# Optimization experiments

Measured on AMD Instinct MI355X. Metric: run time of the kernel, lower is better.

The kernel has to match this reference:

```python
import jax, jax.numpy as jnp
import numpy as np

B, T, N, D, H = 64, 100, 1000, 128, 8
DK = D // H
TANH_CLIP = 10.0  # standard attention-model logit clipping


def setup_inputs() -> dict:
    key = jax.random.key(0)
    ks = jax.random.split(key, 7)
    embeddings = jax.random.normal(ks[0], (B, N, D), jnp.float32)
    Wkvl = jax.random.normal(ks[1], (D, 3 * D), jnp.float32) * 0.05   # project_node_embeddings
    Wfixed = jax.random.normal(ks[2], (D, D), jnp.float32) * 0.05     # project_fixed_context
    Wctx = jax.random.normal(ks[3], (D, D), jnp.float32) * 0.05       # env context projection
    Wout = jax.random.normal(ks[4], (D, D), jnp.float32) * 0.05       # glimpse output projection
    idx = jax.random.randint(ks[5], (T, B), 0, N, jnp.int32)          # current node per decode step
    action_mask = jax.random.uniform(ks[6], (T, B, N)) > 0.2          # True = feasible
    action_mask = action_mask.at[..., 0].set(True)                    # >=1 feasible action per row
    return {"embeddings": embeddings, "Wkvl": Wkvl, "Wfixed": Wfixed,
            "Wctx": Wctx, "Wout": Wout, "idx": idx, "action_mask": action_mask}


def reference(embeddings, Wkvl, Wfixed, Wctx, Wout, idx, action_mask):
    # ---- _precompute ----
    graph_ctx = embeddings.mean(axis=1) @ Wfixed                      # [B, D]
    gk, gv, lk = jnp.split(embeddings @ Wkvl, 3, axis=-1)             # each [B, N, D]

    # ---- all T decode steps batched (dynamic embeddings are zero / static env) ----
    # NOTE: the source overwrites glimpse_key with glimpse_val (glimpse_key = cached.glimpse_val + dyn)
    # and calls logit_attention(query, glimpse_key, glimpse_key, ...), so keys == values == gv.
    cur = jnp.take_along_axis(embeddings, idx.T[..., None], axis=1)   # [B, T, D] current node embed
    query = graph_ctx[:, None, :] + cur @ Wctx                        # [B, T, D]

    q = query.reshape(B, T, H, DK).transpose(0, 2, 1, 3)              # [B, H, T, dk]
    k = gv.reshape(B, N, H, DK).transpose(0, 2, 1, 3)                 # [B, H, N, dk]
    v = k                                                             # keys == values per source

    infeasible = ~action_mask.transpose(1, 0, 2)                      # [B, T, N]

    # glimpse (inner) attention, masked
    compat = jnp.einsum('bhtd,bhnd->bhtn', q, k) / jnp.sqrt(jnp.float32(DK))
    compat = jnp.where(infeasible[:, None], -jnp.inf, compat)
    attn = jax.nn.softmax(compat, axis=-1)                            # [B, H, T, N]
    glimpse = jnp.einsum('bhtn,bhnd->bthd', attn, v).reshape(B, T, D) @ Wout  # [B, T, D]

    # pointer logits with tanh clipping
    logits = jnp.einsum('btd,bnd->btn', glimpse, lk) / jnp.sqrt(jnp.float32(D))
    logits = TANH_CLIP * jnp.tanh(logits)
    logits = jnp.where(infeasible, -jnp.inf, logits)
    return jax.nn.log_softmax(logits, axis=-1)                        # [B, T, N]
```

## Files before the change

kernel.cpp:

```cpp
#include <hip/hip_runtime.h>
#include <math.h>

#define B_  64
#define T_  100
#define N_  1000
#define NP_ 1024
#define TP_ 112
#define D_  128
#define H_  8
#define DK_ 16

#define NEG_BIG (-1e30f)

#define OFF_GVH  0
#define OFF_LKH  16777216
#define OFF_GVT  33554432
#define OFF_CTX  50331648
#define OFF_QH   50364416
#define OFF_GPH  52199424
#define OFF_WT   53837824
#define OFF_WV   53870592
#define OFF_WCT  53936128
#define OFF_PART 53968896
#define OFF_PM   54231040
#define OFF_OPT  55148544
#define OFF_LP   62488576

typedef __attribute__((ext_vector_type(8))) short short8;
typedef __attribute__((ext_vector_type(4))) short bs4;
typedef __attribute__((ext_vector_type(4))) float f32x4;

#if __has_builtin(__builtin_amdgcn_mfma_f32_16x16x16bf16_1k)
#define MFMA16(a, b, c) __builtin_amdgcn_mfma_f32_16x16x16bf16_1k(a, b, c, 0, 0, 0)
#else
__device__ __forceinline__ f32x4 mfma16_asm(bs4 a, bs4 b, f32x4 c) {
    f32x4 d;
    asm volatile("v_mfma_f32_16x16x16_bf16 %0, %1, %2, %3"
                 : "=v"(d) : "v"(a), "v"(b), "v"(c));
    return d;
}
#define MFMA16(a, b, c) mfma16_asm(a, b, c)
#endif

__device__ __forceinline__ unsigned int f2bf(float f) {
    unsigned int u = __float_as_uint(f);
    return (u + 0x7fffu + ((u >> 16) & 1u)) >> 16;
}
__device__ __forceinline__ unsigned int packbf(float a, float b) {
    return f2bf(a) | (f2bf(b) << 16);
}
__device__ __forceinline__ float bf2f(unsigned short u) {
    return __uint_as_float(((unsigned int)u) << 16);
}

__global__ __launch_bounds__(256) void pre_kernel(
        const float* __restrict__ Wkvl, const float* __restrict__ Wout,
        const float* __restrict__ Wctx, const float* __restrict__ emb,
        const unsigned char* __restrict__ am,
        unsigned short* __restrict__ wv, unsigned short* __restrict__ wt,
        unsigned short* __restrict__ wct, float* __restrict__ part,
        unsigned long long* __restrict__ pm) {
    __shared__ float p2[256];
    int bx = blockIdx.x;
    int tid = threadIdx.x;
    if (bx < 256) {
        int i = bx * 256 + tid;
        if (i < 32768) {
            int n = i >> 7, k = i & 127;
            wv[i] = (unsigned short)f2bf(Wkvl[k * 384 + 128 + n]);
        } else if (i < 49152) {
            int j = i - 32768;
            wt[j] = (unsigned short)f2bf(Wout[(j & 127) * D_ + (j >> 7)]);
        } else {
            int j = i - 49152;
            wct[j] = (unsigned short)f2bf(Wctx[(j & 127) * D_ + (j >> 7)]);
        }
    } else if (bx < 768) {
        int b2 = bx - 256;
        int b = b2 >> 3, c = b2 & 7;
        int d = tid & 127, half = tid >> 7;
        int nstart = c * 125 + (half ? 63 : 0);
        int ncnt = half ? 62 : 63;
        const float* e = emb + ((size_t)b * N_ + nstart) * D_ + d;
        float s = 0.f;
        for (int n = 0; n < ncnt; ++n) s += e[(size_t)n * D_];
        p2[tid] = s;
        __syncthreads();
        if (half == 0) part[((size_t)b * 8 + c) * D_ + d] = p2[d] + p2[d + 128];
    } else {
        int rid = bx - 768;
        int t = rid >> 6;
        int wvx = tid >> 6, lane = tid & 63;
        const unsigned char* amrow = am + (size_t)rid * N_;
        unsigned long long* pmrow = pm + (size_t)rid * 16;
        #pragma unroll
        for (int i = 0; i < 4; ++i) {
            int c = wvx * 4 + i;
            int n = c * 64 + lane;
            unsigned char v = (t < T_ && n < N_) ? amrow[n] : (unsigned char)0;
            unsigned long long mb = __ballot(v != 0);
            if (lane == 0) pmrow[c] = mb;
        }
    }
}

__global__ __launch_bounds__(128) void ctxb_kernel(
        const float* __restrict__ part, const float* __restrict__ Wfixed,
        float* __restrict__ ctx) {
    __shared__ float mean[D_];
    int b = blockIdx.x;
    int d = threadIdx.x;
    float s = 0.f;
    for (int c = 0; c < 8; ++c) s += part[((size_t)b * 8 + c) * D_ + d];
    mean[d] = s * (1.0f / N_);
    __syncthreads();
    float acc = 0.f;
    for (int k = 0; k < D_; ++k) acc += mean[k] * Wfixed[k * D_ + d];
    ctx[b * D_ + d] = acc;
}

__global__ __launch_bounds__(256) void proj_kernel(
        const float* __restrict__ emb, const unsigned short* __restrict__ wv,
        unsigned short* __restrict__ gvh, unsigned short* __restrict__ lkh,
        unsigned short* __restrict__ gvT) {
    __shared__ unsigned short As[64 * 136];
    __shared__ unsigned short Gs[64 * 130];
    int rb = blockIdx.x;
    int tid = threadIdx.x;
    int w = tid >> 6, lane = tid & 63, col = lane & 15, quad = lane >> 4;
    const float* a0 = emb + (size_t)rb * 64 * D_;
    #pragma unroll
    for (int i = 0; i < 8; ++i) {
        int idx = tid + i * 256;
        int r = idx >> 5, kq = idx & 31;
        float4 f = *(const float4*)(a0 + r * D_ + kq * 4);
        *(uint2*)&As[r * 136 + kq * 4] = make_uint2(packbf(f.x, f.y), packbf(f.z, f.w));
    }
    __syncthreads();
    short8 bfr[4][4];
    #pragma unroll
    for (int i = 0; i < 4; ++i) {
        int ncol = i * 64 + w * 16 + col;
        #pragma unroll
        for (int kq = 0; kq < 4; ++kq)
            bfr[i][kq] = *(const short8*)(wv + (size_t)ncol * D_ + kq * 32 + quad * 8);
    }
    #pragma unroll
    for (int mt = 0; mt < 4; ++mt) {
        short8 af[4];
        #pragma unroll
        for (int kq = 0; kq < 4; ++kq)
            af[kq] = *(const short8*)&As[(mt * 16 + col) * 136 + kq * 32 + quad * 8];
        size_t base[4];
        #pragma unroll
        for (int r = 0; r < 4; ++r) {
            int m = rb * 64 + mt * 16 + quad * 4 + r;
            int bb = m / N_;
            int nn = m - bb * N_;
            base[r] = ((size_t)bb * NP_ + nn) * D_;
        }
        #pragma unroll
        for (int i = 0; i < 4; ++i) {
            f32x4 acc = {0.f, 0.f, 0.f, 0.f};
            #pragma unroll
            for (int kq = 0; kq < 4; ++kq)
                acc = __builtin_amdgcn_mfma_f32_16x16x32_bf16(af[kq], bfr[i][kq], acc, 0, 0, 0);
            int ncol = i * 64 + w * 16 + col;
            unsigned short* dst = (ncol < 128) ? gvh : lkh;
            int cc = ncol & 127;
            #pragma unroll
            for (int r = 0; r < 4; ++r) {
                unsigned short hv = (unsigned short)f2bf(acc[r]);
                dst[base[r] + cc] = hv;
                if (ncol < 128)
                    Gs[(mt * 16 + quad * 4 + r) * 130 + ncol] = hv;
            }
        }
    }
    __syncthreads();
    #pragma unroll
    for (int it = 0; it < 32; ++it) {
        int idx = tid + it * 256;
        int d = idx >> 6, nl = idx & 63;
        int m = rb * 64 + nl;
        int bb = m / N_, nn = m - bb * N_;
        gvT[((size_t)bb * D_ + d) * NP_ + nn] = Gs[nl * 130 + d];
    }
}

__global__ __launch_bounds__(256) void query_kernel(
        const float* __restrict__ emb, const unsigned short* __restrict__ wct,
        const float* __restrict__ ctx, const int* __restrict__ idxp,
        unsigned short* __restrict__ qh) {
    __shared__ unsigned short As[64 * 136];
    int blk = blockIdx.x;
    int tid = threadIdx.x;
    int w = tid >> 6, lane = tid & 63, col = lane & 15, quad = lane >> 4;
    #pragma unroll
    for (int i = 0; i < 8; ++i) {
        int idx = tid + i * 256;
        int r = idx >> 5, kq = idx & 31;
        int gr = blk * 64 + r;
        int b = gr / T_, t = gr - b * T_;
        int node = idxp[t * B_ + b];
        float4 f = *(const float4*)(emb + ((size_t)b * N_ + node) * D_ + kq * 4);
        *(uint2*)&As[r * 136 + kq * 4] = make_uint2(packbf(f.x, f.y), packbf(f.z, f.w));
    }
    __syncthreads();
    short8 bfr[2][4];
    #pragma unroll
    for (int i = 0; i < 2; ++i) {
        int ncol = (w * 2 + i) * 16 + col;
        #pragma unroll
        for (int kq = 0; kq < 4; ++kq)
            bfr[i][kq] = *(const short8*)(wct + (size_t)ncol * D_ + kq * 32 + quad * 8);
    }
    #pragma unroll
    for (int mt = 0; mt < 4; ++mt) {
        short8 af[4];
        #pragma unroll
        for (int kq = 0; kq < 4; ++kq)
            af[kq] = *(const short8*)&As[(mt * 16 + col) * 136 + kq * 32 + quad * 8];
        int bb[4], tt_[4];
        #pragma unroll
        for (int r = 0; r < 4; ++r) {
            int gr = blk * 64 + mt * 16 + quad * 4 + r;
            bb[r] = gr / T_; tt_[r] = gr - bb[r] * T_;
        }
        #pragma unroll
        for (int i = 0; i < 2; ++i) {
            f32x4 acc = {0.f, 0.f, 0.f, 0.f};
            #pragma unroll
            for (int kq = 0; kq < 4; ++kq)
                acc = __builtin_amdgcn_mfma_f32_16x16x32_bf16(af[kq], bfr[i][kq], acc, 0, 0, 0);
            int ncol = (w * 2 + i) * 16 + col;
            #pragma unroll
            for (int r = 0; r < 4; ++r) {
                float v = (acc[r] + ctx[bb[r] * D_ + ncol]) * 0.25f;
                qh[((size_t)bb[r] * TP_ + tt_[r]) * D_ + ncol] = (unsigned short)f2bf(v);
            }
        }
    }
}

__global__ __launch_bounds__(512) void attn_part_kernel(
        const unsigned short* __restrict__ gvh, const unsigned short* __restrict__ gvT,
        const unsigned short* __restrict__ qh, const unsigned int* __restrict__ pm32,
        unsigned short* __restrict__ oPartT, float* __restrict__ lPart) {
    int b = blockIdx.x >> 2;
    int slice = blockIdx.x & 3;
    int tid = threadIdx.x;
    int h = tid >> 6, lane = tid & 63;
    int col = lane & 15, quad = lane >> 4;
    int nbase = slice * 256;

    const unsigned short* gvb  = gvh + (size_t)b * NP_ * D_;
    const unsigned short* gvtb = gvT + (size_t)b * D_ * NP_;

    bs4 ka[16], va[16];
    #pragma unroll
    for (int ch = 0; ch < 16; ++ch) {
        int n0 = nbase + ch * 16;
        ka[ch] = *(const bs4*)(gvb + (size_t)(n0 + col) * D_ + h * DK_ + quad * 4);
        va[ch] = *(const bs4*)(gvtb + (size_t)(h * DK_ + col) * NP_ + n0 + quad * 4);
    }

    for (int bt = 0; bt < 7; ++bt) {
        int t0 = bt * 16;
        bs4 qb = *(const bs4*)(qh + ((size_t)b * TP_ + t0 + col) * D_ + h * DK_ + quad * 4);
        const unsigned int* pmrow = pm32 + ((size_t)(t0 + col) * B_ + b) * 32;
        f32x4 oacc = {0.f, 0.f, 0.f, 0.f};
        float lacc = 0.f;
        #pragma unroll
        for (int ch = 0; ch < 16; ++ch) {
            int bitpos = nbase + ch * 16 + quad * 4;
            unsigned int mw = pmrow[bitpos >> 5] >> (bitpos & 31);
            f32x4 z = {0.f, 0.f, 0.f, 0.f};
            f32x4 st = MFMA16(ka[ch], qb, z);
            float e[4];
            #pragma unroll
            for (int r = 0; r < 4; ++r) {
                e[r] = ((mw >> r) & 1u) ? __expf(st[r]) : 0.f;
                lacc += e[r];
            }
            bs4 pb = { (short)f2bf(e[0]), (short)f2bf(e[1]),
                       (short)f2bf(e[2]), (short)f2bf(e[3]) };
            oacc = MFMA16(va[ch], pb, oacc);
        }
        size_t rec = (size_t)(b * 7 + bt) * 4 + slice;
        unsigned short* op = oPartT + rec * 2048;
        float l = lacc;
        l += __shfl_xor(l, 16);
        l += __shfl_xor(l, 32);
        if (lane < 16) lPart[rec * 128 + col * 8 + h] = l;
        #pragma unroll
        for (int r = 0; r < 4; ++r)
            op[(h * DK_ + quad * 4 + r) * 16 + col] = (unsigned short)f2bf(oacc[r]);
    }
}

__global__ __launch_bounds__(256) void attn_comb_kernel(
        const unsigned short* __restrict__ oPartT, const float* __restrict__ lPart,
        const unsigned short* __restrict__ woutT, unsigned short* __restrict__ gph) {
    __shared__ float lsum[16][8];
    __shared__ unsigned short gl[16][144];
    int bx = blockIdx.x;
    int b = bx / 7, bt = bx - b * 7;
    int t0 = bt * 16;
    int tid = threadIdx.x;
    int w = tid >> 6, lane = tid & 63, col = lane & 15, quad = lane >> 4;

    if (tid < 128) {
        int t = tid >> 3, h = tid & 7;
        float l = 0.f;
        #pragma unroll
        for (int s = 0; s < 4; ++s)
            l += lPart[((size_t)bx * 4 + s) * 128 + t * 8 + h];
        lsum[t][h] = l;
    }
    __syncthreads();
    #pragma unroll
    for (int i = 0; i < 8; ++i) {
        int idx = tid + i * 256;
        int d = idx >> 4, t = idx & 15;
        float s = 0.f;
        #pragma unroll
        for (int sl = 0; sl < 4; ++sl)
            s += bf2f(oPartT[((size_t)bx * 4 + sl) * 2048 + idx]);
        gl[t][d] = (unsigned short)f2bf(s / lsum[t][d >> 4]);
    }
    __syncthreads();
    short8 ga[4];
    #pragma unroll
    for (int kq = 0; kq < 4; ++kq)
        ga[kq] = *(const short8*)&gl[col][kq * 32 + quad * 8];
    #pragma unroll
    for (int dt = 0; dt < 2; ++dt) {
        int dob = w * 32 + dt * 16;
        f32x4 od = {0.f, 0.f, 0.f, 0.f};
        #pragma unroll
        for (int kq = 0; kq < 4; ++kq) {
            short8 wb = *(const short8*)(woutT + (size_t)(dob + col) * D_ + kq * 32 + quad * 8);
            od = __builtin_amdgcn_mfma_f32_16x16x32_bf16(ga[kq], wb, od, 0, 0, 0);
        }
        #pragma unroll
        for (int r = 0; r < 4; ++r) {
            int t = t0 + quad * 4 + r;
            if (t < T_)
                gph[((size_t)b * T_ + t) * D_ + dob + col] = (unsigned short)f2bf(od[r]);
        }
    }
}

__global__ __launch_bounds__(512) void logits_lsm_kernel(
        const unsigned short* __restrict__ gph, const unsigned short* __restrict__ lkh,
        const unsigned char* __restrict__ am, float* __restrict__ outp) {
    __shared__ unsigned short gs[16 * 136];
    __shared__ float lsP[8][17];
    int bx = blockIdx.x;
    int xcd = bx & 7, slot = bx >> 3;
    int b = (slot / 7) * 8 + xcd;
    int bt = slot - (slot / 7) * 7;
    int t0 = bt * 16;
    int tid = threadIdx.x;
    int w = tid >> 6, lane = tid & 63, col = lane & 15, quad = lane >> 4;

    {
        int r = tid >> 5, c = tid & 31;
        int t = t0 + r; if (t > T_ - 1) t = T_ - 1;
        *(uint2*)&gs[r * 136 + c * 4] =
            *(const uint2*)(gph + ((size_t)b * T_ + t) * D_ + c * 4);
    }
    __syncthreads();

    short8 af[4];
    #pragma unroll
    for (int kq = 0; kq < 4; ++kq)
        af[kq] = *(const short8*)&gs[col * 136 + kq * 32 + quad * 8];

    const unsigned short* lkb = lkh + (size_t)b * NP_ * D_;
    const float rsc = 0.08838834764831845f;
    float y[8][4];
    float es[4] = {0.f, 0.f, 0.f, 0.f};
    #pragma unroll
    for (int i = 0; i < 8; ++i) {
        int n = w * 128 + i * 16 + col;
        f32x4 acc = {0.f, 0.f, 0.f, 0.f};
        #pragma unroll
        for (int kq = 0; kq < 4; ++kq) {
            short8 bf = *(const short8*)(lkb + (size_t)n * D_ + kq * 32 + quad * 8);
            acc = __builtin_amdgcn_mfma_f32_16x16x32_bf16(af[kq], bf, acc, 0, 0, 0);
        }
        bool vn = n < N_;
        #pragma unroll
        for (int r = 0; r < 4; ++r) {
            int t = t0 + quad * 4 + r;
            float yv = fminf(fmaxf(2.f * (acc[r] * rsc), -60.f), 60.f);
            float ex = __expf(yv);
            float th = 10.f * (ex - 1.f) / (ex + 1.f);
            bool feas = (t < T_) && vn &&
                        (am[((size_t)t * B_ + b) * N_ + (vn ? n : 0)] != 0);
            y[i][r] = feas ? th : NEG_BIG;
            es[r] += feas ? __expf(th - 10.f) : 0.f;
        }
    }
    #pragma unroll
    for (int r = 0; r < 4; ++r) {
        float s = es[r];
        s += __shfl_xor(s, 1); s += __shfl_xor(s, 2);
        s += __shfl_xor(s, 4); s += __shfl_xor(s, 8);
        es[r] = s;
    }
    if (col == 0) {
        #pragma unroll
        for (int r = 0; r < 4; ++r) lsP[w][quad * 4 + r] = es[r];
    }
    __syncthreads();
    float lse[4];
    #pragma unroll
    for (int r = 0; r < 4; ++r) {
        int tl = quad * 4 + r;
        float s = 0.f;
        #pragma unroll
        for (int ww = 0; ww < 8; ++ww) s += lsP[ww][tl];
        lse[r] = 10.f + logf(s);
    }
    #pragma unroll
    for (int i = 0; i < 8; ++i) {
        int n = w * 128 + i * 16 + col;
        if (n < N_) {
            #pragma unroll
            for (int r = 0; r < 4; ++r) {
                int t = t0 + quad * 4 + r;
                if (t < T_)
                    outp[((size_t)b * T_ + t) * N_ + n] = y[i][r] - lse[r];
            }
        }
    }
}

extern "C" void kernel_launch(void* const* d_in, const int* in_sizes, int n_in,
                              void* d_out, int out_size, void* d_ws, size_t ws_size,
                              hipStream_t stream) {
    const float* emb    = (const float*)d_in[0];
    const float* Wkvl   = (const float*)d_in[1];
    const float* Wfixed = (const float*)d_in[2];
    const float* Wctx   = (const float*)d_in[3];
    const float* Wout   = (const float*)d_in[4];
    const int*   idxp   = (const int*)d_in[5];
    const unsigned char* am = (const unsigned char*)d_in[6];

    char* ws = (char*)d_ws;
    unsigned short* gvh  = (unsigned short*)(ws + OFF_GVH);
    unsigned short* lkh  = (unsigned short*)(ws + OFF_LKH);
    unsigned short* gvT  = (unsigned short*)(ws + OFF_GVT);
    float*          ctx  = (float*)(ws + OFF_CTX);
    unsigned short* qh   = (unsigned short*)(ws + OFF_QH);
    unsigned short* gph  = (unsigned short*)(ws + OFF_GPH);
    unsigned short* wt   = (unsigned short*)(ws + OFF_WT);
    unsigned short* wv   = (unsigned short*)(ws + OFF_WV);
    unsigned short* wct  = (unsigned short*)(ws + OFF_WCT);
    float*          part = (float*)(ws + OFF_PART);
    unsigned long long* pm = (unsigned long long*)(ws + OFF_PM);
    unsigned short* opt  = (unsigned short*)(ws + OFF_OPT);
    float*          lP   = (float*)(ws + OFF_LP);
    float*          outp = (float*)d_out;

    pre_kernel      <<<dim3(7936), dim3(256), 0, stream>>>(Wkvl, Wout, Wctx, emb, am,
                                                           wv, wt, wct, part, pm);
    ctxb_kernel     <<<dim3(64),   dim3(128), 0, stream>>>(part, Wfixed, ctx);
    proj_kernel     <<<dim3(1000), dim3(256), 0, stream>>>(emb, wv, gvh, lkh, gvT);
    query_kernel    <<<dim3(100),  dim3(256), 0, stream>>>(emb, wct, ctx, idxp, qh);
    attn_part_kernel<<<dim3(256),  dim3(512), 0, stream>>>(gvh, gvT, qh,
                                                           (const unsigned int*)pm, opt, lP);
    attn_comb_kernel<<<dim3(448),  dim3(256), 0, stream>>>(opt, lP, wt, gph);
    logits_lsm_kernel<<<dim3(448), dim3(512), 0, stream>>>(gph, lkh, am, outp);
}
```

Before: 220.0 us.

## Fuse mean reduction into projection, drop gvT transpose, merge combine with logits

The embedding mean is now computed as per-block partial sums inside the projection kernel while the tile is already loaded, and the context matmul moves into the query kernel. This removes the separate emb re-read in pre_kernel and the ctxb launch. The transposed gv copy is no longer written; attention instead gathers V values with strided scalar loads from gvh. The attention combine and Wout projection are fused into the logits/log-softmax kernel, which drops the gph round trip and one launch. The cost is redundant Wfixed matvecs per query block and less efficient V loads.

```diff
diff --git a/kernel.cpp b/kernel.cpp
--- a/kernel.cpp
+++ b/kernel.cpp
@@ -14,17 +14,14 @@
 
 #define OFF_GVH  0
 #define OFF_LKH  16777216
-#define OFF_GVT  33554432
-#define OFF_CTX  50331648
-#define OFF_QH   50364416
-#define OFF_GPH  52199424
-#define OFF_WT   53837824
-#define OFF_WV   53870592
-#define OFF_WCT  53936128
-#define OFF_PART 53968896
-#define OFF_PM   54231040
-#define OFF_OPT  55148544
-#define OFF_LP   62488576
+#define OFF_P2   33554432
+#define OFF_QH   34603008
+#define OFF_WT   36438016
+#define OFF_WV   36470784
+#define OFF_WCT  36536320
+#define OFF_PM   36569088
+#define OFF_OPT  37486592
+#define OFF_LP   44826624
 
 typedef __attribute__((ext_vector_type(8))) short short8;
 typedef __attribute__((ext_vector_type(4))) short bs4;
@@ -55,12 +52,9 @@
 
 __global__ __launch_bounds__(256) void pre_kernel(
         const float* __restrict__ Wkvl, const float* __restrict__ Wout,
-        const float* __restrict__ Wctx, const float* __restrict__ emb,
-        const unsigned char* __restrict__ am,
+        const float* __restrict__ Wctx, const unsigned char* __restrict__ am,
         unsigned short* __restrict__ wv, unsigned short* __restrict__ wt,
-        unsigned short* __restrict__ wct, float* __restrict__ part,
-        unsigned long long* __restrict__ pm) {
-    __shared__ float p2[256];
+        unsigned short* __restrict__ wct, unsigned long long* __restrict__ pm) {
     int bx = blockIdx.x;
     int tid = threadIdx.x;
     if (bx < 256) {
@@ -75,20 +69,8 @@
             int j = i - 49152;
             wct[j] = (unsigned short)f2bf(Wctx[(j & 127) * D_ + (j >> 7)]);
         }
-    } else if (bx < 768) {
-        int b2 = bx - 256;
-        int b = b2 >> 3, c = b2 & 7;
-        int d = tid & 127, half = tid >> 7;
-        int nstart = c * 125 + (half ? 63 : 0);
-        int ncnt = half ? 62 : 63;
-        const float* e = emb + ((size_t)b * N_ + nstart) * D_ + d;
-        float s = 0.f;
-        for (int n = 0; n < ncnt; ++n) s += e[(size_t)n * D_];
-        p2[tid] = s;
-        __syncthreads();
-        if (half == 0) part[((size_t)b * 8 + c) * D_ + d] = p2[d] + p2[d + 128];
     } else {
-        int rid = bx - 768;
+        int rid = bx - 256;
         int t = rid >> 6;
         int wvx = tid >> 6, lane = tid & 63;
         const unsigned char* amrow = am + (size_t)rid * N_;
@@ -104,39 +86,50 @@
     }
 }
 
-__global__ __launch_bounds__(128) void ctxb_kernel(
-        const float* __restrict__ part, const float* __restrict__ Wfixed,
-        float* __restrict__ ctx) {
-    __shared__ float mean[D_];
-    int b = blockIdx.x;
-    int d = threadIdx.x;
-    float s = 0.f;
-    for (int c = 0; c < 8; ++c) s += part[((size_t)b * 8 + c) * D_ + d];
-    mean[d] = s * (1.0f / N_);
-    __syncthreads();
-    float acc = 0.f;
-    for (int k = 0; k < D_; ++k) acc += mean[k] * Wfixed[k * D_ + d];
-    ctx[b * D_ + d] = acc;
-}
-
 __global__ __launch_bounds__(256) void proj_kernel(
         const float* __restrict__ emb, const unsigned short* __restrict__ wv,
         unsigned short* __restrict__ gvh, unsigned short* __restrict__ lkh,
-        unsigned short* __restrict__ gvT) {
+        float* __restrict__ part2) {
     __shared__ unsigned short As[64 * 136];
-    __shared__ unsigned short Gs[64 * 130];
+    __shared__ float csA[8][132];
+    __shared__ float csB[8][132];
     int rb = blockIdx.x;
     int tid = threadIdx.x;
     int w = tid >> 6, lane = tid & 63, col = lane & 15, quad = lane >> 4;
     const float* a0 = emb + (size_t)rb * 64 * D_;
+    int b0 = (rb * 64) / N_;
+    int rsplit = (b0 + 1) * N_ - rb * 64;
+    float sa0 = 0.f, sa1 = 0.f, sa2 = 0.f, sa3 = 0.f;
+    float sb0 = 0.f, sb1 = 0.f, sb2 = 0.f, sb3 = 0.f;
     #pragma unroll
     for (int i = 0; i < 8; ++i) {
         int idx = tid + i * 256;
         int r = idx >> 5, kq = idx & 31;
         float4 f = *(const float4*)(a0 + r * D_ + kq * 4);
         *(uint2*)&As[r * 136 + kq * 4] = make_uint2(packbf(f.x, f.y), packbf(f.z, f.w));
-    }
-    __syncthreads();
+        if (r < rsplit) { sa0 += f.x; sa1 += f.y; sa2 += f.z; sa3 += f.w; }
+        else            { sb0 += f.x; sb1 += f.y; sb2 += f.z; sb3 += f.w; }
+    }
+    {
+        int g = tid >> 5, kq = tid & 31;
+        csA[g][kq * 4 + 0] = sa0; csA[g][kq * 4 + 1] = sa1;
+        csA[g][kq * 4 + 2] = sa2; csA[g][kq * 4 + 3] = sa3;
+        csB[g][kq * 4 + 0] = sb0; csB[g][kq * 4 + 1] = sb1;
+        csB[g][kq * 4 + 2] = sb2; csB[g][kq * 4 + 3] = sb3;
+    }
+    __syncthreads();
+    if (tid < 128) {
+        float s = 0.f;
+        #pragma unroll
+        for (int g = 0; g < 8; ++g) s += csA[g][tid];
+        part2[((size_t)rb * 2) * 128 + tid] = s;
+    } else {
+        int d = tid - 128;
+        float s = 0.f;
+        #pragma unroll
+        for (int g = 0; g < 8; ++g) s += csB[g][d];
+        part2[((size_t)rb * 2 + 1) * 128 + d] = s;
+    }
     short8 bfr[4][4];
     #pragma unroll
     for (int i = 0; i < 4; ++i) {
@@ -169,33 +162,24 @@
             unsigned short* dst = (ncol < 128) ? gvh : lkh;
             int cc = ncol & 127;
             #pragma unroll
-            for (int r = 0; r < 4; ++r) {
-                unsigned short hv = (unsigned short)f2bf(acc[r]);
-                dst[base[r] + cc] = hv;
-                if (ncol < 128)
-                    Gs[(mt * 16 + quad * 4 + r) * 130 + ncol] = hv;
-            }
-        }
-    }
-    __syncthreads();
-    #pragma unroll
-    for (int it = 0; it < 32; ++it) {
-        int idx = tid + it * 256;
-        int d = idx >> 6, nl = idx & 63;
-        int m = rb * 64 + nl;
-        int bb = m / N_, nn = m - bb * N_;
-        gvT[((size_t)bb * D_ + d) * NP_ + nn] = Gs[nl * 130 + d];
+            for (int r = 0; r < 4; ++r)
+                dst[base[r] + cc] = (unsigned short)f2bf(acc[r]);
+        }
     }
 }
 
 __global__ __launch_bounds__(256) void query_kernel(
         const float* __restrict__ emb, const unsigned short* __restrict__ wct,
-        const float* __restrict__ ctx, const int* __restrict__ idxp,
-        unsigned short* __restrict__ qh) {
+        const float* __restrict__ part2, const float* __restrict__ Wfixed,
+        const int* __restrict__ idxp, unsigned short* __restrict__ qh) {
     __shared__ unsigned short As[64 * 136];
+    __shared__ float means[2][128];
+    __shared__ float ctx_s[2][132];
     int blk = blockIdx.x;
     int tid = threadIdx.x;
     int w = tid >> 6, lane = tid & 63, col = lane & 15, quad = lane >> 4;
+    int bA = (blk * 64) / T_;
+    int bB = (blk * 64 + 63) / T_;
     #pragma unroll
     for (int i = 0; i < 8; ++i) {
         int idx = tid + i * 256;
@@ -206,6 +190,26 @@
         float4 f = *(const float4*)(emb + ((size_t)b * N_ + node) * D_ + kq * 4);
         *(uint2*)&As[r * 136 + kq * 4] = make_uint2(packbf(f.x, f.y), packbf(f.z, f.w));
     }
+    {
+        int half = tid >> 7, d = tid & 127;
+        int bq = half ? bB : bA;
+        int r0 = (bq * N_) >> 6;
+        int r1 = (bq * N_ + N_ - 1) >> 6;
+        float s = 0.f;
+        for (int rb = r0; rb <= r1; ++rb) {
+            int sel = ((rb * 64) / N_ == bq) ? 0 : 1;
+            s += part2[((size_t)rb * 2 + sel) * 128 + d];
+        }
+        means[half][d] = s * (1.0f / N_);
+    }
+    __syncthreads();
+    {
+        int half = tid >> 7, d = tid & 127;
+        float acc = 0.f;
+        for (int k = 0; k < D_; ++k)
+            acc += means[half][k] * Wfixed[(size_t)k * D_ + d];
+        ctx_s[half][d] = acc;
+    }
     __syncthreads();
     short8 bfr[2][4];
     #pragma unroll
@@ -236,7 +240,7 @@
             int ncol = (w * 2 + i) * 16 + col;
             #pragma unroll
             for (int r = 0; r < 4; ++r) {
-                float v = (acc[r] + ctx[bb[r] * D_ + ncol]) * 0.25f;
+                float v = (acc[r] + ctx_s[bb[r] - bA][ncol]) * 0.25f;
                 qh[((size_t)bb[r] * TP_ + tt_[r]) * D_ + ncol] = (unsigned short)f2bf(v);
             }
         }
@@ -244,8 +248,8 @@
 }
 
 __global__ __launch_bounds__(512) void attn_part_kernel(
-        const unsigned short* __restrict__ gvh, const unsigned short* __restrict__ gvT,
-        const unsigned short* __restrict__ qh, const unsigned int* __restrict__ pm32,
+        const unsigned short* __restrict__ gvh, const unsigned short* __restrict__ qh,
+        const unsigned int* __restrict__ pm32,
         unsigned short* __restrict__ oPartT, float* __restrict__ lPart) {
     int b = blockIdx.x >> 2;
     int slice = blockIdx.x & 3;
@@ -254,15 +258,18 @@
     int col = lane & 15, quad = lane >> 4;
     int nbase = slice * 256;
 
-    const unsigned short* gvb  = gvh + (size_t)b * NP_ * D_;
-    const unsigned short* gvtb = gvT + (size_t)b * D_ * NP_;
+    const unsigned short* gvb = gvh + (size_t)b * NP_ * D_;
 
     bs4 ka[16], va[16];
     #pragma unroll
     for (int ch = 0; ch < 16; ++ch) {
         int n0 = nbase + ch * 16;
         ka[ch] = *(const bs4*)(gvb + (size_t)(n0 + col) * D_ + h * DK_ + quad * 4);
-        va[ch] = *(const bs4*)(gvtb + (size_t)(h * DK_ + col) * NP_ + n0 + quad * 4);
+        bs4 vv;
+        #pragma unroll
+        for (int j = 0; j < 4; ++j)
+            vv[j] = (short)gvb[(size_t)(n0 + quad * 4 + j) * D_ + h * DK_ + col];
+        va[ch] = vv;
     }
 
     for (int bt = 0; bt < 7; ++bt) {
@@ -299,63 +306,13 @@
     }
 }
 
-__global__ __launch_bounds__(256) void attn_comb_kernel(
+__global__ __launch_bounds__(512) void final_kernel(
         const unsigned short* __restrict__ oPartT, const float* __restrict__ lPart,
-        const unsigned short* __restrict__ woutT, unsigned short* __restrict__ gph) {
+        const unsigned short* __restrict__ woutT, const unsigned short* __restrict__ lkh,
+        const unsigned char* __restrict__ am, float* __restrict__ outp) {
     __shared__ float lsum[16][8];
     __shared__ unsigned short gl[16][144];
-    int bx = blockIdx.x;
-    int b = bx / 7, bt = bx - b * 7;
-    int t0 = bt * 16;
-    int tid = threadIdx.x;
-    int w = tid >> 6, lane = tid & 63, col = lane & 15, quad = lane >> 4;
-
-    if (tid < 128) {
-        int t = tid >> 3, h = tid & 7;
-        float l = 0.f;
-        #pragma unroll
-        for (int s = 0; s < 4; ++s)
-            l += lPart[((size_t)bx * 4 + s) * 128 + t * 8 + h];
-        lsum[t][h] = l;
-    }
-    __syncthreads();
-    #pragma unroll
-    for (int i = 0; i < 8; ++i) {
-        int idx = tid + i * 256;
-        int d = idx >> 4, t = idx & 15;
-        float s = 0.f;
-        #pragma unroll
-        for (int sl = 0; sl < 4; ++sl)
-            s += bf2f(oPartT[((size_t)bx * 4 + sl) * 2048 + idx]);
-        gl[t][d] = (unsigned short)f2bf(s / lsum[t][d >> 4]);
-    }
-    __syncthreads();
-    short8 ga[4];
-    #pragma unroll
-    for (int kq = 0; kq < 4; ++kq)
-        ga[kq] = *(const short8*)&gl[col][kq * 32 + quad * 8];
-    #pragma unroll
-    for (int dt = 0; dt < 2; ++dt) {
-        int dob = w * 32 + dt * 16;
-        f32x4 od = {0.f, 0.f, 0.f, 0.f};
-        #pragma unroll
-        for (int kq = 0; kq < 4; ++kq) {
-            short8 wb = *(const short8*)(woutT + (size_t)(dob + col) * D_ + kq * 32 + quad * 8);
-            od = __builtin_amdgcn_mfma_f32_16x16x32_bf16(ga[kq], wb, od, 0, 0, 0);
-        }
-        #pragma unroll
-        for (int r = 0; r < 4; ++r) {
-            int t = t0 + quad * 4 + r;
-            if (t < T_)
-                gph[((size_t)b * T_ + t) * D_ + dob + col] = (unsigned short)f2bf(od[r]);
-        }
-    }
-}
-
-__global__ __launch_bounds__(512) void logits_lsm_kernel(
-        const unsigned short* __restrict__ gph, const unsigned short* __restrict__ lkh,
-        const unsigned char* __restrict__ am, float* __restrict__ outp) {
-    __shared__ unsigned short gs[16 * 136];
+    __shared__ unsigned short gs[16][136];
     __shared__ float lsP[8][17];
     int bx = blockIdx.x;
     int xcd = bx & 7, slot = bx >> 3;
@@ -364,19 +321,50 @@
     int t0 = bt * 16;
     int tid = threadIdx.x;
     int w = tid >> 6, lane = tid & 63, col = lane & 15, quad = lane >> 4;
-
+    size_t rec0 = (size_t)(b * 7 + bt) * 4;
+
+    if (tid < 128) {
+        int t = tid >> 3, hh = tid & 7;
+        float l = 0.f;
+        #pragma unroll
+        for (int s = 0; s < 4; ++s)
+            l += lPart[(rec0 + s) * 128 + t * 8 + hh];
+        lsum[t][hh] = l;
+    }
+    __syncthreads();
+    #pragma unroll
+    for (int i = 0; i < 4; ++i) {
+        int idx = tid + i * 512;
+        int d = idx >> 4, t = idx & 15;
+        float s = 0.f;
+        #pragma unroll
+        for (int sl = 0; sl < 4; ++sl)
+            s += bf2f(oPartT[(rec0 + sl) * 2048 + idx]);
+        gl[t][d] = (unsigned short)f2bf(s / lsum[t][d >> 4]);
+    }
+    __syncthreads();
     {
-        int r = tid >> 5, c = tid & 31;
-        int t = t0 + r; if (t > T_ - 1) t = T_ - 1;
-        *(uint2*)&gs[r * 136 + c * 4] =
-            *(const uint2*)(gph + ((size_t)b * T_ + t) * D_ + c * 4);
+        short8 ga[4];
+        #pragma unroll
+        for (int kq = 0; kq < 4; ++kq)
+            ga[kq] = *(const short8*)&gl[col][kq * 32 + quad * 8];
+        int dob = w * 16;
+        f32x4 od = {0.f, 0.f, 0.f, 0.f};
+        #pragma unroll
+        for (int kq = 0; kq < 4; ++kq) {
+            short8 wb = *(const short8*)(woutT + (size_t)(dob + col) * D_ + kq * 32 + quad * 8);
+            od = __builtin_amdgcn_mfma_f32_16x16x32_bf16(ga[kq], wb, od, 0, 0, 0);
+        }
+        #pragma unroll
+        for (int r = 0; r < 4; ++r)
+            gs[quad * 4 + r][dob + col] = (unsigned short)f2bf(od[r]);
     }
     __syncthreads();
 
     short8 af[4];
     #pragma unroll
     for (int kq = 0; kq < 4; ++kq)
-        af[kq] = *(const short8*)&gs[col * 136 + kq * 32 + quad * 8];
+        af[kq] = *(const short8*)&gs[col][kq * 32 + quad * 8];
 
     const unsigned short* lkb = lkh + (size_t)b * NP_ * D_;
     const float rsc = 0.08838834764831845f;
@@ -453,26 +441,22 @@
     char* ws = (char*)d_ws;
     unsigned short* gvh  = (unsigned short*)(ws + OFF_GVH);
     unsigned short* lkh  = (unsigned short*)(ws + OFF_LKH);
-    unsigned short* gvT  = (unsigned short*)(ws + OFF_GVT);
-    float*          ctx  = (float*)(ws + OFF_CTX);
+    float*          p2   = (float*)(ws + OFF_P2);
     unsigned short* qh   = (unsigned short*)(ws + OFF_QH);
-    unsigned short* gph  = (unsigned short*)(ws + OFF_GPH);
     unsigned short* wt   = (unsigned short*)(ws + OFF_WT);
     unsigned short* wv   = (unsigned short*)(ws + OFF_WV);
     unsigned short* wct  = (unsigned short*)(ws + OFF_WCT);
-    float*          part = (float*)(ws + OFF_PART);
     unsigned long long* pm = (unsigned long long*)(ws + OFF_PM);
     unsigned short* opt  = (unsigned short*)(ws + OFF_OPT);
     float*          lP   = (float*)(ws + OFF_LP);
     float*          outp = (float*)d_out;
 
-    pre_kernel      <<<dim3(7936), dim3(256), 0, stream>>>(Wkvl, Wout, Wctx, emb, am,
-                                                           wv, wt, wct, part, pm);
-    ctxb_kernel     <<<dim3(64),   dim3(128), 0, stream>>>(part, Wfixed, ctx);
-    proj_kernel     <<<dim3(1000), dim3(256), 0, stream>>>(emb, wv, gvh, lkh, gvT);
-    query_kernel    <<<dim3(100),  dim3(256), 0, stream>>>(emb, wct, ctx, idxp, qh);
-    attn_part_kernel<<<dim3(256),  dim3(512), 0, stream>>>(gvh, gvT, qh,
+    pre_kernel      <<<dim3(7424), dim3(256), 0, stream>>>(Wkvl, Wout, Wctx, am,
+                                                           wv, wt, wct, pm);
+    proj_kernel     <<<dim3(1000), dim3(256), 0, stream>>>(emb, wv, gvh, lkh, p2);
+    query_kernel    <<<dim3(100),  dim3(256), 0, stream>>>(emb, wct, p2, Wfixed,
+                                                           idxp, qh);
+    attn_part_kernel<<<dim3(256),  dim3(512), 0, stream>>>(gvh, qh,
                                                            (const unsigned int*)pm, opt, lP);
-    attn_comb_kernel<<<dim3(448),  dim3(256), 0, stream>>>(opt, lP, wt, gph);
-    logits_lsm_kernel<<<dim3(448), dim3(512), 0, stream>>>(gph, lkh, am, outp);
-}
+    final_kernel    <<<dim3(448),  dim3(512), 0, stream>>>(opt, lP, wt, lkh, am, outp);
+}
```

Result: faster. 190.5 us (-13.4%).
